# Kernel optimization log

Hardware: AMD Instinct MI355X
Metric: run time of the kernel (lower is better)

## Reference

```python
import jax, jax.numpy as jnp
import numpy as np

K = 3  # spatial window (window_size = [1,3,3,1])


def _extract_patches(x, k):
    """TF-style extract_patches, VALID padding, stride 1, rate 1.
    x: [B,H,W,C] -> [B,Ho,Wo,k*k*C] with depth ordering (ki, kj, c)."""
    B, H, W, C = x.shape
    Ho, Wo = H - k + 1, W - k + 1
    cols = [x[:, ki:ki + Ho, kj:kj + Wo, :] for ki in range(k) for kj in range(k)]
    return jnp.concatenate(cols, axis=-1)


def setup_inputs() -> dict:
    key = jax.random.key(0)
    k1, k2 = jax.random.split(key)
    x = jax.random.normal(k1, (8, 32, 32, 32), dtype=jnp.float32)
    # weight shape per build(): (1, 1, 1, K*K*C, filters) = (1,1,1,288,64)
    w = jax.random.normal(k2, (1, 1, 1, 3 * 3 * 32, 64), dtype=jnp.float32) * 0.05
    bias = jnp.zeros((64,), dtype=jnp.float32)
    return {"x": x, "w": w, "bias": bias}


def reference(x, w, bias):
    # patches: [B,Ho,Wo,KKC]
    p = _extract_patches(x, K)
    # broadcast add: [B,Ho,Wo,KKC,1] + [KKC,F] -> [B,Ho,Wo,KKC,F]
    r = p[..., None] + w[0, 0, 0]
    # tropical conv: max-plus minus min-plus over the patch axis, plus bias
    return jnp.max(r, axis=3) - jnp.min(r, axis=3) + bias
```

## Files before the change

### kernel.cpp

```cpp
#include <hip/hip_runtime.h>
#include <math.h>


typedef _Float16 half2v __attribute__((ext_vector_type(2)));
typedef _Float16 half8v __attribute__((ext_vector_type(8)));

#define WSTRIDE 296

__device__ __forceinline__ half2v h2(unsigned u) {
  return __builtin_bit_cast(half2v, u);
}
__device__ __forceinline__ unsigned u32(half2v h) {
  return __builtin_bit_cast(unsigned, h);
}
__device__ __forceinline__ void tap(half2v a, half2v& mx, half2v& mn) {
  mx = __builtin_elementwise_max(mx, a);
  mn = __builtin_elementwise_min(mn, a);
}

__global__ __launch_bounds__(256, 3) void trop_kernel(
    const float* __restrict__ x, const float* __restrict__ w,
    const float* __restrict__ bias, float* __restrict__ out) {
  __shared__ _Float16 wt[64 * WSTRIDE];
  __shared__ _Float16 xh[3 * 18 * 32];
  __shared__ uint4 red[2][2][2][64];

  const int i = blockIdx.x;
  const int b = blockIdx.y;
  const int z = blockIdx.z;
  const int tid = threadIdx.x;
  const int f = tid & 63;
  const int W = __builtin_amdgcn_readfirstlane(tid >> 6);
  const int p = W & 1;
  const int chalf = W >> 1;
  const int j0 = z * 16 + p * 8;

  {
    const float* wp = w + f;
    const int kb = W * 72;
#pragma unroll
    for (int blk = 0; blk < 9; ++blk) {
      const int k0 = kb + blk * 8;
      half8v v;
#pragma unroll
      for (int u = 0; u < 8; ++u) v[u] = (_Float16)wp[(k0 + u) * 64];
      *(half8v*)&wt[f * WSTRIDE + k0] = v;
    }
  }

  {
    const float* xb = x + (((size_t)b * 32 + i) * 32) * 32;
#pragma unroll
    for (int t = 0; t < 4; ++t) {
      const int g = tid + t * 256;
      if (g < 864) {
        const int ki = g / 288;
        const int rem = g - ki * 288;
        const int col = rem >> 4;
        const int cp = rem & 15;
        int gcol = z * 16 + col;
        if (gcol > 31) gcol = 31;
        const float2 v = *(const float2*)(xb + ki * 1024 + gcol * 32 + cp * 2);
        half2v h;
        h.x = (_Float16)v.x;
        h.y = (_Float16)v.y;
        *(half2v*)&xh[(ki * 18 + col) * 32 + cp * 2] = h;
      }
    }
  }

  __syncthreads();

  const _Float16 NI = (_Float16)(-INFINITY), PI = (_Float16)INFINITY;
  half2v mxi, mni;
  mxi.x = NI; mxi.y = NI;
  mni.x = PI; mni.y = PI;
  half2v mx[8], mn[8];
#pragma unroll
  for (int t = 0; t < 8; ++t) {
    mx[t] = mxi;
    mn[t] = mni;
  }

#pragma clang loop unroll(disable)
  for (int kc = 0; kc < 6; ++kc) {
    const int ki = kc >> 1;
    const int c8 = (chalf << 4) + ((kc & 1) << 3);
    const _Float16* xrow = &xh[(ki * 18 + p * 8) * 32 + c8];
    const _Float16* wrow = &wt[f * WSTRIDE + ki * 96 + c8];

    uint4 xa[10];
#pragma unroll
    for (int t = 0; t < 10; ++t) xa[t] = *(const uint4*)&xrow[t * 32];
    const uint4 wa0 = *(const uint4*)&wrow[0];
    const uint4 wa1 = *(const uint4*)&wrow[32];
    const uint4 wa2 = *(const uint4*)&wrow[64];

#define DOD(D)                                      \
  {                                                 \
    const half2v w0 = h2(wa0.D);                    \
    const half2v w1 = h2(wa1.D);                    \
    const half2v w2 = h2(wa2.D);                    \
    _Pragma("unroll") for (int t = 0; t < 8; ++t) { \
      tap(h2(xa[t].D) + w0, mx[t], mn[t]);          \
      tap(h2(xa[t + 1].D) + w1, mx[t], mn[t]);      \
      tap(h2(xa[t + 2].D) + w2, mx[t], mn[t]);      \
    }                                               \
  }
    DOD(x) DOD(y) DOD(z) DOD(w)
#undef DOD
  }

  if (chalf == 1) {
    uint4 t0, t1;
    t0.x = u32(mx[0]); t0.y = u32(mx[1]); t0.z = u32(mx[2]); t0.w = u32(mx[3]);
    t1.x = u32(mx[4]); t1.y = u32(mx[5]); t1.z = u32(mx[6]); t1.w = u32(mx[7]);
    red[p][0][0][f] = t0;
    red[p][0][1][f] = t1;
    t0.x = u32(mn[0]); t0.y = u32(mn[1]); t0.z = u32(mn[2]); t0.w = u32(mn[3]);
    t1.x = u32(mn[4]); t1.y = u32(mn[5]); t1.z = u32(mn[6]); t1.w = u32(mn[7]);
    red[p][1][0][f] = t0;
    red[p][1][1][f] = t1;
  }
  __syncthreads();
  if (chalf == 0) {
    const uint4 a0 = red[p][0][0][f], a1 = red[p][0][1][f];
    const uint4 b0 = red[p][1][0][f], b1 = red[p][1][1][f];
    mx[0] = __builtin_elementwise_max(mx[0], h2(a0.x));
    mx[1] = __builtin_elementwise_max(mx[1], h2(a0.y));
    mx[2] = __builtin_elementwise_max(mx[2], h2(a0.z));
    mx[3] = __builtin_elementwise_max(mx[3], h2(a0.w));
    mx[4] = __builtin_elementwise_max(mx[4], h2(a1.x));
    mx[5] = __builtin_elementwise_max(mx[5], h2(a1.y));
    mx[6] = __builtin_elementwise_max(mx[6], h2(a1.z));
    mx[7] = __builtin_elementwise_max(mx[7], h2(a1.w));
    mn[0] = __builtin_elementwise_min(mn[0], h2(b0.x));
    mn[1] = __builtin_elementwise_min(mn[1], h2(b0.y));
    mn[2] = __builtin_elementwise_min(mn[2], h2(b0.z));
    mn[3] = __builtin_elementwise_min(mn[3], h2(b0.w));
    mn[4] = __builtin_elementwise_min(mn[4], h2(b1.x));
    mn[5] = __builtin_elementwise_min(mn[5], h2(b1.y));
    mn[6] = __builtin_elementwise_min(mn[6], h2(b1.z));
    mn[7] = __builtin_elementwise_min(mn[7], h2(b1.w));

    const float bv = bias[f];
    float* ob = out + (((size_t)b * 30 + i) * 30 + j0) * 64 + f;
#pragma unroll
    for (int t = 0; t < 8; ++t) {
      if (j0 + t < 30) {
        ob[t * 64] = fmaxf((float)mx[t].x, (float)mx[t].y) -
                     fminf((float)mn[t].x, (float)mn[t].y) + bv;
      }
    }
  }
}

extern "C" void kernel_launch(void* const* d_in, const int* in_sizes, int n_in,
                              void* d_out, int out_size, void* d_ws, size_t ws_size,
                              hipStream_t stream) {
  const float* x = (const float*)d_in[0];
  const float* w = (const float*)d_in[1];
  const float* bias = (const float*)d_in[2];
  float* out = (float*)d_out;
  dim3 grid(30, 8, 2);
  dim3 block(256);
  hipLaunchKernelGGL(trop_kernel, grid, block, 0, stream, x, w, bias, out);
}
```

Baseline: 68.71 us.

## Merge column halves into 1024-thread blocks with 4-way channel split and reduction

Each block now covers a full output row (all 30 columns) with 1024 threads: 4 column groups times 4 channel quarters, instead of two z-blocks of 256 threads. Each weight is converted to fp16 once per block in a new packed layout, which halves the redundant per-block weight staging. The shared-memory buffer is reused for a 4-way cross-wave max/min reduction. In exchange the grid shrinks to 240 large blocks, there is an extra barrier, and occupancy granularity becomes coarser.

Measured after the change: 66.18 us. 3.7% less time.

```diff
diff --git a/kernel.cpp b/kernel.cpp
--- a/kernel.cpp
+++ b/kernel.cpp
@@ -3,9 +3,6 @@
 
 
 typedef _Float16 half2v __attribute__((ext_vector_type(2)));
-typedef _Float16 half8v __attribute__((ext_vector_type(8)));
-
-#define WSTRIDE 296
 
 __device__ __forceinline__ half2v h2(unsigned u) {
   return __builtin_bit_cast(half2v, u);
@@ -13,135 +10,149 @@
 __device__ __forceinline__ unsigned u32(half2v h) {
   return __builtin_bit_cast(unsigned, h);
 }
-__device__ __forceinline__ void tap(half2v a, half2v& mx, half2v& mn) {
+__device__ __forceinline__ void tap1(half2v a, half2v& mx, half2v& mn) {
   mx = __builtin_elementwise_max(mx, a);
   mn = __builtin_elementwise_min(mn, a);
 }
 
-__global__ __launch_bounds__(256, 3) void trop_kernel(
+__global__ __launch_bounds__(1024) void trop_kernel(
     const float* __restrict__ x, const float* __restrict__ w,
     const float* __restrict__ bias, float* __restrict__ out) {
-  __shared__ _Float16 wt[64 * WSTRIDE];
-  __shared__ _Float16 xh[3 * 18 * 32];
-  __shared__ uint4 red[2][2][2][64];
+  __shared__ __align__(16) unsigned char smem[49152];
+  _Float16* const wt2 = (_Float16*)smem;
+  _Float16* const xh = (_Float16*)(smem + 36864);
 
   const int i = blockIdx.x;
   const int b = blockIdx.y;
-  const int z = blockIdx.z;
   const int tid = threadIdx.x;
   const int f = tid & 63;
   const int W = __builtin_amdgcn_readfirstlane(tid >> 6);
-  const int p = W & 1;
-  const int chalf = W >> 1;
-  const int j0 = z * 16 + p * 8;
+  const int cg = W & 3;
+  const int q = W >> 2;
+  const int j0 = cg * 8;
 
-  {
-    const float* wp = w + f;
-    const int kb = W * 72;
 #pragma unroll
-    for (int blk = 0; blk < 9; ++blk) {
-      const int k0 = kb + blk * 8;
-      half8v v;
-#pragma unroll
-      for (int u = 0; u < 8; ++u) v[u] = (_Float16)wp[(k0 + u) * 64];
-      *(half8v*)&wt[f * WSTRIDE + k0] = v;
+  for (int it = 0; it < 3; ++it) {
+    const int idx = tid + it * 1024;
+    if (idx < 2304) {
+      const int ff = idx & 63;
+      const int rest = idx >> 6;
+      const int qq = rest & 3;
+      const int tp = rest >> 2;
+      const float* wp = w + (size_t)((tp * 32 + qq * 8) * 64 + ff);
+      half2v h01, h23, h45, h67;
+      h01.x = (_Float16)wp[0 * 64]; h01.y = (_Float16)wp[1 * 64];
+      h23.x = (_Float16)wp[2 * 64]; h23.y = (_Float16)wp[3 * 64];
+      h45.x = (_Float16)wp[4 * 64]; h45.y = (_Float16)wp[5 * 64];
+      h67.x = (_Float16)wp[6 * 64]; h67.y = (_Float16)wp[7 * 64];
+      uint4 pk;
+      pk.x = u32(h01); pk.y = u32(h23); pk.z = u32(h45); pk.w = u32(h67);
+      *(uint4*)&wt2[(size_t)((tp * 4 + qq) * 64 + ff) * 8] = pk;
     }
   }
 
   {
     const float* xb = x + (((size_t)b * 32 + i) * 32) * 32;
 #pragma unroll
-    for (int t = 0; t < 4; ++t) {
-      const int g = tid + t * 256;
-      if (g < 864) {
-        const int ki = g / 288;
-        const int rem = g - ki * 288;
+    for (int t = 0; t < 2; ++t) {
+      const int g = tid + t * 1024;
+      if (g < 1536) {
+        const int ki = g >> 9;
+        const int rem = g & 511;
         const int col = rem >> 4;
         const int cp = rem & 15;
-        int gcol = z * 16 + col;
-        if (gcol > 31) gcol = 31;
-        const float2 v = *(const float2*)(xb + ki * 1024 + gcol * 32 + cp * 2);
+        const float2 v = *(const float2*)(xb + ki * 1024 + col * 32 + cp * 2);
         half2v h;
         h.x = (_Float16)v.x;
         h.y = (_Float16)v.y;
-        *(half2v*)&xh[(ki * 18 + col) * 32 + cp * 2] = h;
+        *(half2v*)&xh[(ki * 32 + col) * 32 + cp * 2] = h;
       }
     }
   }
 
   __syncthreads();
 
+  int cc[10];
+#pragma unroll
+  for (int u = 0; u < 10; ++u) {
+    const int col = (j0 + u < 32) ? (j0 + u) : 31;
+    cc[u] = col * 32 + q * 8;
+  }
+
   const _Float16 NI = (_Float16)(-INFINITY), PI = (_Float16)INFINITY;
-  half2v mxi, mni;
-  mxi.x = NI; mxi.y = NI;
-  mni.x = PI; mni.y = PI;
   half2v mx[8], mn[8];
 #pragma unroll
   for (int t = 0; t < 8; ++t) {
-    mx[t] = mxi;
-    mn[t] = mni;
+    mx[t].x = NI; mx[t].y = NI;
+    mn[t].x = PI; mn[t].y = PI;
   }
 
 #pragma clang loop unroll(disable)
-  for (int kc = 0; kc < 6; ++kc) {
-    const int ki = kc >> 1;
-    const int c8 = (chalf << 4) + ((kc & 1) << 3);
-    const _Float16* xrow = &xh[(ki * 18 + p * 8) * 32 + c8];
-    const _Float16* wrow = &wt[f * WSTRIDE + ki * 96 + c8];
-
+  for (int ki = 0; ki < 3; ++ki) {
+    const _Float16* xr = &xh[ki * 1024];
+    const _Float16* wr = &wt2[(size_t)((ki * 12 + q) * 64 + f) * 8];
     uint4 xa[10];
 #pragma unroll
-    for (int t = 0; t < 10; ++t) xa[t] = *(const uint4*)&xrow[t * 32];
-    const uint4 wa0 = *(const uint4*)&wrow[0];
-    const uint4 wa1 = *(const uint4*)&wrow[32];
-    const uint4 wa2 = *(const uint4*)&wrow[64];
+    for (int u = 0; u < 10; ++u) xa[u] = *(const uint4*)&xr[cc[u]];
+    const uint4 wk0 = *(const uint4*)&wr[0];
+    const uint4 wk1 = *(const uint4*)&wr[4 * 64 * 8];
+    const uint4 wk2 = *(const uint4*)&wr[8 * 64 * 8];
 
 #define DOD(D)                                      \
   {                                                 \
-    const half2v w0 = h2(wa0.D);                    \
-    const half2v w1 = h2(wa1.D);                    \
-    const half2v w2 = h2(wa2.D);                    \
+    const half2v w0 = h2(wk0.D);                    \
+    const half2v w1 = h2(wk1.D);                    \
+    const half2v w2 = h2(wk2.D);                    \
     _Pragma("unroll") for (int t = 0; t < 8; ++t) { \
-      tap(h2(xa[t].D) + w0, mx[t], mn[t]);          \
-      tap(h2(xa[t + 1].D) + w1, mx[t], mn[t]);      \
-      tap(h2(xa[t + 2].D) + w2, mx[t], mn[t]);      \
+      tap1(h2(xa[t].D) + w0, mx[t], mn[t]);         \
+      tap1(h2(xa[t + 1].D) + w1, mx[t], mn[t]);     \
+      tap1(h2(xa[t + 2].D) + w2, mx[t], mn[t]);     \
     }                                               \
   }
     DOD(x) DOD(y) DOD(z) DOD(w)
 #undef DOD
   }
 
-  if (chalf == 1) {
-    uint4 t0, t1;
-    t0.x = u32(mx[0]); t0.y = u32(mx[1]); t0.z = u32(mx[2]); t0.w = u32(mx[3]);
-    t1.x = u32(mx[4]); t1.y = u32(mx[5]); t1.z = u32(mx[6]); t1.w = u32(mx[7]);
-    red[p][0][0][f] = t0;
-    red[p][0][1][f] = t1;
-    t0.x = u32(mn[0]); t0.y = u32(mn[1]); t0.z = u32(mn[2]); t0.w = u32(mn[3]);
-    t1.x = u32(mn[4]); t1.y = u32(mn[5]); t1.z = u32(mn[6]); t1.w = u32(mn[7]);
-    red[p][1][0][f] = t0;
-    red[p][1][1][f] = t1;
+  __syncthreads();
+  uint4(*red)[4][4][64] = (uint4(*)[4][4][64])smem;
+
+  if (q > 0) {
+    uint4 a;
+    a.x = u32(mx[0]); a.y = u32(mx[1]); a.z = u32(mx[2]); a.w = u32(mx[3]);
+    red[q - 1][cg][0][f] = a;
+    a.x = u32(mx[4]); a.y = u32(mx[5]); a.z = u32(mx[6]); a.w = u32(mx[7]);
+    red[q - 1][cg][1][f] = a;
+    a.x = u32(mn[0]); a.y = u32(mn[1]); a.z = u32(mn[2]); a.w = u32(mn[3]);
+    red[q - 1][cg][2][f] = a;
+    a.x = u32(mn[4]); a.y = u32(mn[5]); a.z = u32(mn[6]); a.w = u32(mn[7]);
+    red[q - 1][cg][3][f] = a;
   }
   __syncthreads();
-  if (chalf == 0) {
-    const uint4 a0 = red[p][0][0][f], a1 = red[p][0][1][f];
-    const uint4 b0 = red[p][1][0][f], b1 = red[p][1][1][f];
-    mx[0] = __builtin_elementwise_max(mx[0], h2(a0.x));
-    mx[1] = __builtin_elementwise_max(mx[1], h2(a0.y));
-    mx[2] = __builtin_elementwise_max(mx[2], h2(a0.z));
-    mx[3] = __builtin_elementwise_max(mx[3], h2(a0.w));
-    mx[4] = __builtin_elementwise_max(mx[4], h2(a1.x));
-    mx[5] = __builtin_elementwise_max(mx[5], h2(a1.y));
-    mx[6] = __builtin_elementwise_max(mx[6], h2(a1.z));
-    mx[7] = __builtin_elementwise_max(mx[7], h2(a1.w));
-    mn[0] = __builtin_elementwise_min(mn[0], h2(b0.x));
-    mn[1] = __builtin_elementwise_min(mn[1], h2(b0.y));
-    mn[2] = __builtin_elementwise_min(mn[2], h2(b0.z));
-    mn[3] = __builtin_elementwise_min(mn[3], h2(b0.w));
-    mn[4] = __builtin_elementwise_min(mn[4], h2(b1.x));
-    mn[5] = __builtin_elementwise_min(mn[5], h2(b1.y));
-    mn[6] = __builtin_elementwise_min(mn[6], h2(b1.z));
-    mn[7] = __builtin_elementwise_min(mn[7], h2(b1.w));
+
+  if (q == 0) {
+#pragma unroll
+    for (int qq = 0; qq < 3; ++qq) {
+      const uint4 a0 = red[qq][cg][0][f];
+      const uint4 a1 = red[qq][cg][1][f];
+      const uint4 b0 = red[qq][cg][2][f];
+      const uint4 b1 = red[qq][cg][3][f];
+      mx[0] = __builtin_elementwise_max(mx[0], h2(a0.x));
+      mx[1] = __builtin_elementwise_max(mx[1], h2(a0.y));
+      mx[2] = __builtin_elementwise_max(mx[2], h2(a0.z));
+      mx[3] = __builtin_elementwise_max(mx[3], h2(a0.w));
+      mx[4] = __builtin_elementwise_max(mx[4], h2(a1.x));
+      mx[5] = __builtin_elementwise_max(mx[5], h2(a1.y));
+      mx[6] = __builtin_elementwise_max(mx[6], h2(a1.z));
+      mx[7] = __builtin_elementwise_max(mx[7], h2(a1.w));
+      mn[0] = __builtin_elementwise_min(mn[0], h2(b0.x));
+      mn[1] = __builtin_elementwise_min(mn[1], h2(b0.y));
+      mn[2] = __builtin_elementwise_min(mn[2], h2(b0.z));
+      mn[3] = __builtin_elementwise_min(mn[3], h2(b0.w));
+      mn[4] = __builtin_elementwise_min(mn[4], h2(b1.x));
+      mn[5] = __builtin_elementwise_min(mn[5], h2(b1.y));
+      mn[6] = __builtin_elementwise_min(mn[6], h2(b1.z));
+      mn[7] = __builtin_elementwise_min(mn[7], h2(b1.w));
+    }
 
     const float bv = bias[f];
     float* ob = out + (((size_t)b * 30 + i) * 30 + j0) * 64 + f;
@@ -162,7 +173,7 @@
   const float* w = (const float*)d_in[1];
   const float* bias = (const float*)d_in[2];
   float* out = (float*)d_out;
-  dim3 grid(30, 8, 2);
-  dim3 block(256);
+  dim3 grid(30, 8);
+  dim3 block(1024);
   hipLaunchKernelGGL(trop_kernel, grid, block, 0, stream, x, w, bias, out);
 }
```
